# Performance work log

Hardware: AMD Instinct MI355X
Metric: run time of the kernel (lower is better)

Reference implementation:

```python
import jax, jax.numpy as jnp
import numpy as np

NUM_HEADS = 16
NUM_LANDMARKS = 64
N_ITER = 6


def iterative_inv(mat):
    # mat: (B, H, L, L) row-stochastic kernel; Newton-Schulz-style iteration
    L = mat.shape[-1]
    I = jnp.eye(L, dtype=mat.dtype)
    K = mat
    # init: V = K^T / max_j(sum_i K_ij)
    denom = jnp.max(jnp.sum(K, axis=-2), axis=-1)[:, :, None, None]
    Vm = (1.0 / denom) * jnp.swapaxes(K, -1, -2)
    for _ in range(N_ITER):
        KV = jnp.matmul(K, Vm)
        Vm = jnp.matmul(0.25 * Vm, 13.0 * I - jnp.matmul(KV, 15.0 * I - jnp.matmul(KV, 7.0 * I - KV)))
    return Vm


def setup_inputs() -> dict:
    key = jax.random.key(0)
    kq, kk, kv = jax.random.split(key, 3)
    B, N, C = 4, 4096, 1024
    return {
        "Q": jax.random.normal(kq, (B, N, C), dtype=jnp.float32),
        "K": jax.random.normal(kk, (B, N, C), dtype=jnp.float32),
        "V": jax.random.normal(kv, (B, N, C), dtype=jnp.float32),
    }


def reference(Q, K, V):
    B, N, C = Q.shape
    H, Lm = NUM_HEADS, NUM_LANDMARKS
    hd = C // H
    scale = hd ** 0.5
    # (B, H, N, hd)
    q = Q.reshape(B, N, H, hd).transpose(0, 2, 1, 3) / scale
    k = K.reshape(B, N, H, hd).transpose(0, 2, 1, 3)
    v = V.reshape(B, N, H, hd).transpose(0, 2, 1, 3)

    # landmark pooling (N divisible by Lm): mean over segments of length N//Lm
    seg = N // Lm
    k_lm = k.reshape(B, H, Lm, seg, hd).mean(axis=-2)  # (B,H,Lm,hd)
    q_lm = q.reshape(B, H, Lm, seg, hd).mean(axis=-2)  # (B,H,Lm,hd)

    kernel_1 = jax.nn.softmax(jnp.einsum('bhnd,bhld->bhnl', q, k_lm), axis=-1)   # (B,H,N,Lm)
    kernel_2 = jax.nn.softmax(jnp.einsum('bhmd,bhld->bhml', q_lm, k_lm), axis=-1)  # (B,H,Lm,Lm)
    kernel_3 = jax.nn.softmax(jnp.einsum('bhld,bhnd->bhln', q_lm, k), axis=-1)   # (B,H,Lm,N)

    out = jnp.matmul(jnp.matmul(kernel_1, iterative_inv(kernel_2)), jnp.matmul(kernel_3, v))
    return out.transpose(0, 2, 1, 3).reshape(B, N, C)
```

## Files before the change

### kernel.cpp

```cpp
#include <hip/hip_runtime.h>
#include <math.h>

#define BB 4
#define NN 4096
#define CC 1024
#define HH 16
#define HD 64
#define LM 64
#define SEG 64
#define BHN (BB*HH)
#define MATP 68
#define MATE (64*MATP)

typedef __attribute__((ext_vector_type(8))) short bf16x8;
typedef __attribute__((ext_vector_type(4))) short s16x4;
typedef __attribute__((ext_vector_type(4))) float f32x4;

__device__ __forceinline__ float shfl_sum16(float v) {
  v += __shfl_xor(v, 1, 16);
  v += __shfl_xor(v, 2, 16);
  v += __shfl_xor(v, 4, 16);
  v += __shfl_xor(v, 8, 16);
  return v;
}

__device__ __forceinline__ void split8(const float* f, bf16x8& hi, bf16x8& lo) {
#pragma unroll
  for (int i = 0; i < 8; ++i) {
    unsigned u = __builtin_bit_cast(unsigned, f[i]);
    float hf = __builtin_bit_cast(float, u & 0xFFFF0000u);
    hi[i] = (short)(u >> 16);
    float l = f[i] - hf;
    unsigned ul = __builtin_bit_cast(unsigned, l);
    lo[i] = (short)(ul >> 16);
  }
}

__device__ __forceinline__ void split4(const float* f, s16x4& hi, s16x4& lo) {
#pragma unroll
  for (int i = 0; i < 4; ++i) {
    unsigned u = __builtin_bit_cast(unsigned, f[i]);
    float hf = __builtin_bit_cast(float, u & 0xFFFF0000u);
    hi[i] = (short)(u >> 16);
    float l = f[i] - hf;
    unsigned ul = __builtin_bit_cast(unsigned, l);
    lo[i] = (short)(ul >> 16);
  }
}

__device__ __forceinline__ int planeAddr(int row, int cd) {
  int B = (row << 7) + (cd << 4);
  return B ^ ((row & 7) << 4);
}
__device__ __forceinline__ bf16x8 ldP(const short* __restrict__ P, int row, int cd) {
  return *(const bf16x8*)((const char*)P + planeAddr(row, cd));
}

__device__ __forceinline__ void xpose4(float x[4], int lane) {
  bool p1 = (lane >> 4) & 1;
  float s0 = p1 ? x[0] : x[1], s1 = p1 ? x[2] : x[3];
  float r0 = __shfl_xor(s0, 16, 64), r1 = __shfl_xor(s1, 16, 64);
  if (p1) { x[0] = r0; x[2] = r1; } else { x[1] = r0; x[3] = r1; }
  bool p2 = (lane >> 5) & 1;
  s0 = p2 ? x[0] : x[2]; s1 = p2 ? x[1] : x[3];
  r0 = __shfl_xor(s0, 32, 64); r1 = __shfl_xor(s1, 32, 64);
  if (p2) { x[0] = r0; x[1] = r1; } else { x[2] = r0; x[3] = r1; }
}

__global__ __launch_bounds__(256) void lm_kernel(
    const float* __restrict__ Q, const float* __restrict__ K,
    float* __restrict__ qlm, float* __restrict__ klm) {
  int bh = blockIdx.y; int b = bh >> 4; int h = bh & 15;
  int tid = threadIdx.x;
  int l = blockIdx.x * 4 + (tid >> 6);
  int d = tid & 63;
  const float* qbase = Q + ((size_t)b*NN + (size_t)l*SEG)*CC + h*HD + d;
  const float* kbase = K + ((size_t)b*NN + (size_t)l*SEG)*CC + h*HD + d;
  float sq = 0.f, sk = 0.f;
#pragma unroll 8
  for (int s = 0; s < SEG; ++s) {
    sq += qbase[(size_t)s*CC];
    sk += kbase[(size_t)s*CC];
  }
  qlm[(size_t)bh*4096 + l*64 + d] = sq * (1.0f/(64.0f*8.0f));
  klm[(size_t)bh*4096 + l*64 + d] = sk * (1.0f/64.0f);
}

__global__ __launch_bounds__(256, 3) void k3v_kernel(
    const float* __restrict__ K, const float* __restrict__ V,
    const float* __restrict__ qlm,
    float* __restrict__ S3, float* __restrict__ ACC3) {
  __shared__ alignas(16) short KEh[64*64], KEl[64*64];
  __shared__ alignas(16) short VtH[64*64], VtL[64*64];
  __shared__ alignas(16) float Erow[64*MATP];
  const int bh = blockIdx.y, b = bh >> 4, h = bh & 15;
  const int tile = blockIdx.x, tid = threadIdx.x;
  const int wid = tid >> 6, lane = tid & 63;
  const int lr = lane & 15, lg = lane >> 4;
  const int m0 = wid*16 + lg*4;

  bf16x8 qh[2], ql[2];
#pragma unroll
  for (int ks = 0; ks < 2; ++ks) {
    const float* qp = qlm + (size_t)bh*4096 + (wid*16 + lr)*64 + ks*32 + lg*8;
    float qf[8];
    *(float4*)&qf[0] = *(const float4*)qp;
    *(float4*)&qf[4] = *(const float4*)(qp + 4);
    split8(qf, qh[ks], ql[ks]);
  }

  f32x4 acc2[4];
#pragma unroll
  for (int t = 0; t < 4; ++t) acc2[t] = (f32x4){0.f, 0.f, 0.f, 0.f};
  float srow[4] = {0.f, 0.f, 0.f, 0.f};

  const int rk0 = tid >> 3,        ck = tid & 7;
  const int rk1 = (tid + 256) >> 3;
  const int dV  = 4*lr + lg;

  float4 gk[2][2], gv[4];

#define K3V_LOAD(SUB)                                                          \
  {                                                                            \
    const int n0_ = tile*128 + (SUB)*64;                                       \
    const float* kb0 = &K[((size_t)b*NN + n0_ + rk0)*CC + h*HD + ck*8];        \
    const float* kb1 = &K[((size_t)b*NN + n0_ + rk1)*CC + h*HD + ck*8];        \
    gk[0][0] = *(const float4*)kb0;  gk[0][1] = *(const float4*)(kb0 + 4);     \
    gk[1][0] = *(const float4*)kb1;  gk[1][1] = *(const float4*)(kb1 + 4);     \
    _Pragma("unroll")                                                          \
    for (int q = 0; q < 4; ++q) {                                              \
      int f = tid + 256*q;                                                     \
      int r = f >> 4, c4 = (f & 15) << 2;                                      \
      gv[q] = *(const float4*)&V[((size_t)b*NN + n0_ + r)*CC + h*HD + c4];     \
    }                                                                          \
  }

#define K3V_WRITE()                                                            \
  {                                                                            \
    _Pragma("unroll")                                                          \
    for (int q2 = 0; q2 < 2; ++q2) {                                           \
      float kf[8];                                                             \
      *(float4*)&kf[0] = gk[q2][0];                                            \
      *(float4*)&kf[4] = gk[q2][1];                                            \
      bf16x8 khv, klv; split8(kf, khv, klv);                                   \
      int r = q2 ? rk1 : rk0;                                                  \
      int A = planeAddr(r, ck);                                                \
      *(bf16x8*)((char*)KEh + A) = khv;                                        \
      *(bf16x8*)((char*)KEl + A) = klv;                                        \
    }                                                                          \
    _Pragma("unroll")                                                          \
    for (int q = 0; q < 4; ++q) {                                              \
      float x[4] = {gv[q].x, gv[q].y, gv[q].z, gv[q].w};                       \
      xpose4(x, lane);                                                         \
      int nb = 16*q + 4*wid;                                                   \
      s16x4 vh, vl; split4(x, vh, vl);                                         \
      int B = (dV << 7) + (nb << 1);                                           \
      B ^= (dV & 7) << 4;                                                      \
      *(s16x4*)((char*)VtH + B) = vh;                                          \
      *(s16x4*)((char*)VtL + B) = vl;                                          \
    }                                                                          \
  }

#define K3V_COMPUTE()                                                          \
  {                                                                            \
    f32x4 zacc[4];                                                             \
    _Pragma("unroll")                                                          \
    for (int t = 0; t < 4; ++t) zacc[t] = (f32x4){0.f, 0.f, 0.f, 0.f};        \
    _Pragma("unroll")                                                          \
    for (int ks = 0; ks < 2; ++ks) {                                           \
      _Pragma("unroll")                                                        \
      for (int tn = 0; tn < 4; ++tn) {                                         \
        bf16x8 bh_ = ldP(KEh, tn*16 + lr, 4*ks + lg);                          \
        bf16x8 bl_ = ldP(KEl, tn*16 + lr, 4*ks + lg);                          \
        zacc[tn] = __builtin_amdgcn_mfma_f32_16x16x32_bf16(qh[ks], bh_, zacc[tn], 0, 0, 0); \
        zacc[tn] = __builtin_amdgcn_mfma_f32_16x16x32_bf16(qh[ks], bl_, zacc[tn], 0, 0, 0); \
        zacc[tn] = __builtin_amdgcn_mfma_f32_16x16x32_bf16(ql[ks], bh_, zacc[tn], 0, 0, 0); \
      }                                                                        \
    }                                                                          \
    float e[4][4];                                                             \
    _Pragma("unroll")                                                          \
    for (int tn = 0; tn < 4; ++tn)                                             \
      _Pragma("unroll")                                                        \
      for (int r = 0; r < 4; ++r) e[tn][r] = __expf(zacc[tn][r]);              \
    _Pragma("unroll")                                                          \
    for (int r = 0; r < 4; ++r) {                                              \
      float t = e[0][r] + e[1][r] + e[2][r] + e[3][r];                         \
      srow[r] += shfl_sum16(t);                                                \
    }                                                                          \
    _Pragma("unroll")                                                          \
    for (int tn = 0; tn < 4; ++tn) {                                           \
      const int n = tn*16 + lr;                                                \
      _Pragma("unroll")                                                        \
      for (int r = 0; r < 4; ++r) Erow[(m0 + r)*MATP + n] = e[tn][r];          \
    }                                                                          \
    _Pragma("unroll")                                                          \
    for (int ks = 0; ks < 2; ++ks) {                                           \
      float fa[8];                                                             \
      const float* ap = Erow + (wid*16 + lr)*MATP + ks*32 + lg*8;              \
      *(float4*)&fa[0] = *(const float4*)ap;                                   \
      *(float4*)&fa[4] = *(const float4*)(ap + 4);                             \
      bf16x8 ah, al; split8(fa, ah, al);                                       \
      _Pragma("unroll")                                                        \
      for (int tn = 0; tn < 4; ++tn) {                                         \
        bf16x8 bh_ = ldP(VtH, tn*16 + lr, 4*ks + lg);                          \
        bf16x8 bl_ = ldP(VtL, tn*16 + lr, 4*ks + lg);                          \
        acc2[tn] = __builtin_amdgcn_mfma_f32_16x16x32_bf16(ah, bh_, acc2[tn], 0, 0, 0); \
        acc2[tn] = __builtin_amdgcn_mfma_f32_16x16x32_bf16(ah, bl_, acc2[tn], 0, 0, 0); \
        acc2[tn] = __builtin_amdgcn_mfma_f32_16x16x32_bf16(al, bh_, acc2[tn], 0, 0, 0); \
      }                                                                        \
    }                                                                          \
  }

  K3V_LOAD(0)
  K3V_WRITE()
  __syncthreads();
  K3V_LOAD(1)
  K3V_COMPUTE()
  __syncthreads();
  K3V_WRITE()
  __syncthreads();
  K3V_COMPUTE()

  if (lr == 0) {
#pragma unroll
    for (int r = 0; r < 4; ++r)
      atomicAdd(&S3[bh*64 + m0 + r], srow[r]);
  }
#pragma unroll
  for (int tn = 0; tn < 4; ++tn)
#pragma unroll
    for (int r = 0; r < 4; ++r)
      atomicAdd(&ACC3[(size_t)bh*4096 + (m0 + r)*64 + tn*16 + lr], acc2[tn][r]);
}

template<bool FUSE, bool HR, bool HC, bool HG>
__device__ __forceinline__ void mm_mfma(
    const float* __restrict__ Arow, const float* __restrict__ Scol,
    float diagc, float scale,
    float* __restrict__ OutRow, float* __restrict__ OutCol, float* __restrict__ OutGlob,
    int wr, int tn, int lane) {
  const int lr = lane & 15, lg = lane >> 4;
  f32x4 acc = (f32x4){0.f, 0.f, 0.f, 0.f};

#pragma unroll
  for (int ks = 0; ks < 2; ++ks) {
    const int kb = ks*32 + lg*8;
    float fa[8];
    const float* ap = Arow + (wr*16 + lr)*MATP + kb;
    *(float4*)&fa[0] = *(const float4*)ap;
    *(float4*)&fa[4] = *(const float4*)(ap + 4);
    bf16x8 ah, al; split8(fa, ah, al);
    float fb[8];
    const float* bp = Scol + (tn*16 + lr)*MATP + kb;
    *(float4*)&fb[0] = *(const float4*)bp;
    *(float4*)&fb[4] = *(const float4*)(bp + 4);
    if (FUSE) {
      int diff = (tn*16 + lr) - kb;
#pragma unroll
      for (int i = 0; i < 8; ++i) fb[i] = (i == diff ? diagc : 0.f) - fb[i];
    }
    bf16x8 bh_, bl_; split8(fb, bh_, bl_);
    acc = __builtin_amdgcn_mfma_f32_16x16x32_bf16(ah, bh_, acc, 0, 0, 0);
    acc = __builtin_amdgcn_mfma_f32_16x16x32_bf16(ah, bl_, acc, 0, 0, 0);
    acc = __builtin_amdgcn_mfma_f32_16x16x32_bf16(al, bh_, acc, 0, 0, 0);
  }
  __syncthreads();
  const int n = tn*16 + lr, m0 = wr*16 + lg*4;
  float v0 = scale*acc[0], v1 = scale*acc[1], v2 = scale*acc[2], v3 = scale*acc[3];
  if (HC) *(float4*)&OutCol[n*MATP + m0] = make_float4(v0, v1, v2, v3);
  if (HR) {
    OutRow[(m0+0)*MATP + n] = v0;
    OutRow[(m0+1)*MATP + n] = v1;
    OutRow[(m0+2)*MATP + n] = v2;
    OutRow[(m0+3)*MATP + n] = v3;
  }
  if (HG) {
    OutGlob[(m0+0)*64 + n] = v0;
    OutGlob[(m0+1)*64 + n] = v1;
    OutGlob[(m0+2)*64 + n] = v2;
    OutGlob[(m0+3)*64 + n] = v3;
  }
  __syncthreads();
}

__global__ __launch_bounds__(1024, 1) void inv_kernel(
    const float* __restrict__ qlm, const float* __restrict__ klm,
    const float* __restrict__ S3, const float* __restrict__ ACC3,
    float* __restrict__ W) {
  extern __shared__ float sm[];
  float* K2row = sm;
  float* Vmrow = sm + 1*MATE;
  float* Vmcol = sm + 2*MATE;
  float* Xrow  = sm + 3*MATE;
  float* Xcol  = sm + 4*MATE;
  float* Ycol  = sm + 5*MATE;
  float* Zcol  = sm + 6*MATE;
  float* rs    = sm + 7*MATE;
  float* rinv  = rs + 256;
  float* red   = rinv + 64;
  const int bh = blockIdx.x, tid = threadIdx.x;
  const int wid = tid >> 6, lane = tid & 63;
  const int wr = wid & 3, tn = wid >> 2;
  const int lr = lane & 15, lg = lane >> 4;
  const int m0 = wr*16 + lg*4, n = tn*16 + lr;

  {
    int f = tid, r = f >> 4, c4 = (f & 15) << 2;
    *(float4*)&Xrow[r*MATP + c4] = *(const float4*)&qlm[(size_t)bh*4096 + f*4];
    *(float4*)&Xcol[r*MATP + c4] = *(const float4*)&klm[(size_t)bh*4096 + f*4];
  }
  __syncthreads();

  {
    f32x4 zacc = (f32x4){0.f, 0.f, 0.f, 0.f};
#pragma unroll
    for (int ks = 0; ks < 2; ++ks) {
      const int kb = ks*32 + lg*8;
      float fa[8];
      const float* ap = Xrow + (wr*16 + lr)*MATP + kb;
      *(float4*)&fa[0] = *(const float4*)ap;
      *(float4*)&fa[4] = *(const float4*)(ap + 4);
      bf16x8 ah, al; split8(fa, ah, al);
      float fb[8];
      const float* bp = Xcol + (tn*16 + lr)*MATP + kb;
      *(float4*)&fb[0] = *(const float4*)bp;
      *(float4*)&fb[4] = *(const float4*)(bp + 4);
      bf16x8 bh_, bl_; split8(fb, bh_, bl_);
      zacc = __builtin_amdgcn_mfma_f32_16x16x32_bf16(ah, bh_, zacc, 0, 0, 0);
      zacc = __builtin_amdgcn_mfma_f32_16x16x32_bf16(ah, bl_, zacc, 0, 0, 0);
      zacc = __builtin_amdgcn_mfma_f32_16x16x32_bf16(al, bh_, zacc, 0, 0, 0);
    }
    float e[4];
#pragma unroll
    for (int r = 0; r < 4; ++r) e[r] = __expf(zacc[r]);
    float part[4];
#pragma unroll
    for (int r = 0; r < 4; ++r) part[r] = shfl_sum16(e[r]);
    if (lr == 0) {
#pragma unroll
      for (int r = 0; r < 4; ++r) rs[(m0 + r)*4 + tn] = part[r];
    }
    __syncthreads();
    if (tid < 64)
      rinv[tid] = 1.0f / (rs[tid*4] + rs[tid*4+1] + rs[tid*4+2] + rs[tid*4+3]);
    __syncthreads();
#pragma unroll
    for (int r = 0; r < 4; ++r)
      K2row[(m0+r)*MATP + n] = e[r] * rinv[m0 + r];
  }
  __syncthreads();

  if (tid < 64) {
    float c = 0.f;
#pragma unroll 8
    for (int i = 0; i < 64; ++i) c += K2row[i*MATP + tid];
#pragma unroll
    for (int m = 1; m < 64; m <<= 1) c = fmaxf(c, __shfl_xor(c, m, 64));
    if (tid == 0) red[0] = 1.0f / c;
  }
  __syncthreads();
  const float invden = red[0];

  {
    int f = tid, i = f >> 4, c4 = (f & 15) << 2;
    float4 kv = *(const float4*)&K2row[i*MATP + c4];
    kv.x *= invden; kv.y *= invden; kv.z *= invden; kv.w *= invden;
    *(float4*)&Vmcol[i*MATP + c4] = kv;
    Vmrow[(c4+0)*MATP + i] = kv.x;
    Vmrow[(c4+1)*MATP + i] = kv.y;
    Vmrow[(c4+2)*MATP + i] = kv.z;
    Vmrow[(c4+3)*MATP + i] = kv.w;
  }
  __syncthreads();

  for (int it = 0; it < 6; ++it) {
    mm_mfma<false, true,  true,  false>(K2row, Vmcol, 0.f,  1.0f,  Xrow, Xcol, nullptr, wr, tn, lane);
    mm_mfma<true,  false, true,  false>(Xrow,  Xcol,  7.f,  1.0f,  nullptr, Ycol, nullptr, wr, tn, lane);
    mm_mfma<true,  false, true,  false>(Xrow,  Ycol,  15.f, 1.0f,  nullptr, Zcol, nullptr, wr, tn, lane);
    mm_mfma<true,  true,  true,  false>(Vmrow, Zcol,  13.f, 0.25f, Vmrow, Vmcol, nullptr, wr, tn, lane);
  }

  {
    int f = tid, k = f >> 4, c4 = (f & 15) << 2;
    float4 tv = *(const float4*)&ACC3[(size_t)bh*4096 + f*4];
    float ri = 1.0f / S3[bh*64 + k];
    Ycol[(c4+0)*MATP + k] = tv.x * ri;
    Ycol[(c4+1)*MATP + k] = tv.y * ri;
    Ycol[(c4+2)*MATP + k] = tv.z * ri;
    Ycol[(c4+3)*MATP + k] = tv.w * ri;
  }
  __syncthreads();
  mm_mfma<false, false, false, true>(Vmrow, Ycol, 0.f, 1.0f, nullptr, nullptr, W + (size_t)bh*4096, wr, tn, lane);
}

__global__ __launch_bounds__(256, 3) void out_kernel(
    const float* __restrict__ Q, const float* __restrict__ klm,
    const float* __restrict__ W, float* __restrict__ Out) {
  __shared__ alignas(16) short KlH[64*64], KlL[64*64];
  __shared__ alignas(16) short WtH[64*64], WtL[64*64];
  __shared__ alignas(16) float Prow[64*MATP];
  const int bh = blockIdx.y, b = bh >> 4, h = bh & 15;
  const int n0 = blockIdx.x * 64;
  const int tid = threadIdx.x;
  const int wid = tid >> 6, lane = tid & 63;
  const int lr = lane & 15, lg = lane >> 4;
  const int m0 = wid*16 + lg*4;

#pragma unroll
  for (int q2 = 0; q2 < 2; ++q2) {
    int f = tid + 256*q2;
    int r = f >> 3, c = f & 7;
    const float* kp = &klm[(size_t)bh*4096 + r*64 + c*8];
    float kf[8];
    *(float4*)&kf[0] = *(const float4*)kp;
    *(float4*)&kf[4] = *(const float4*)(kp + 4);
    bf16x8 khv, klv; split8(kf, khv, klv);
    int A = planeAddr(r, c);
    *(bf16x8*)((char*)KlH + A) = khv;
    *(bf16x8*)((char*)KlL + A) = klv;
  }
  const int dW = 4*lr + lg;
#pragma unroll
  for (int q = 0; q < 4; ++q) {
    int f = tid + 256*q;
    int r = f >> 4, c4 = (f & 15) << 2;
    float4 wv = *(const float4*)&W[(size_t)bh*4096 + r*64 + c4];
    float x[4] = {wv.x, wv.y, wv.z, wv.w};
    xpose4(x, lane);
    int nb = 16*q + 4*wid;
    s16x4 wh, wl; split4(x, wh, wl);
    int B = (dW << 7) + (nb << 1);
    B ^= (dW & 7) << 4;
    *(s16x4*)((char*)WtH + B) = wh;
    *(s16x4*)((char*)WtL + B) = wl;
  }

  bf16x8 qh[2], qlo[2];
#pragma unroll
  for (int ks = 0; ks < 2; ++ks) {
    const float* qp = Q + ((size_t)b*NN + n0 + wid*16 + lr)*CC + h*HD + ks*32 + lg*8;
    float qf[8];
    *(float4*)&qf[0] = *(const float4*)qp;
    *(float4*)&qf[4] = *(const float4*)(qp + 4);
#pragma unroll
    for (int i = 0; i < 8; ++i) qf[i] *= 0.125f;
    split8(qf, qh[ks], qlo[ks]);
  }
  __syncthreads();

  f32x4 zacc[4];
#pragma unroll
  for (int t = 0; t < 4; ++t) zacc[t] = (f32x4){0.f, 0.f, 0.f, 0.f};
#pragma unroll
  for (int ks = 0; ks < 2; ++ks) {
#pragma unroll
    for (int tn = 0; tn < 4; ++tn) {
      bf16x8 bh_ = ldP(KlH, tn*16 + lr, 4*ks + lg);
      bf16x8 bl_ = ldP(KlL, tn*16 + lr, 4*ks + lg);
      zacc[tn] = __builtin_amdgcn_mfma_f32_16x16x32_bf16(qh[ks], bh_, zacc[tn], 0, 0, 0);
      zacc[tn] = __builtin_amdgcn_mfma_f32_16x16x32_bf16(qh[ks], bl_, zacc[tn], 0, 0, 0);
      zacc[tn] = __builtin_amdgcn_mfma_f32_16x16x32_bf16(qlo[ks], bh_, zacc[tn], 0, 0, 0);
    }
  }
  float e[4][4];
#pragma unroll
  for (int tn = 0; tn < 4; ++tn)
#pragma unroll
    for (int r = 0; r < 4; ++r) e[tn][r] = __expf(zacc[tn][r]);
#pragma unroll
  for (int r = 0; r < 4; ++r) {
    float t = e[0][r] + e[1][r] + e[2][r] + e[3][r];
    t = shfl_sum16(t);
    float ri = 1.0f / t;
#pragma unroll
    for (int tn = 0; tn < 4; ++tn) e[tn][r] *= ri;
  }
#pragma unroll
  for (int tn = 0; tn < 4; ++tn) {
    const int n = tn*16 + lr;
#pragma unroll
    for (int r = 0; r < 4; ++r) Prow[(m0+r)*MATP + n] = e[tn][r];
  }

  f32x4 oacc[4];
#pragma unroll
  for (int t = 0; t < 4; ++t) oacc[t] = (f32x4){0.f, 0.f, 0.f, 0.f};
#pragma unroll
  for (int ks = 0; ks < 2; ++ks) {
    float fa[8];
    const float* ap = Prow + (wid*16 + lr)*MATP + ks*32 + lg*8;
    *(float4*)&fa[0] = *(const float4*)ap;
    *(float4*)&fa[4] = *(const float4*)(ap + 4);
    bf16x8 ah, al; split8(fa, ah, al);
#pragma unroll
    for (int tn = 0; tn < 4; ++tn) {
      bf16x8 bh_ = ldP(WtH, tn*16 + lr, 4*ks + lg);
      bf16x8 bl_ = ldP(WtL, tn*16 + lr, 4*ks + lg);
      oacc[tn] = __builtin_amdgcn_mfma_f32_16x16x32_bf16(ah, bh_, oacc[tn], 0, 0, 0);
      oacc[tn] = __builtin_amdgcn_mfma_f32_16x16x32_bf16(ah, bl_, oacc[tn], 0, 0, 0);
      oacc[tn] = __builtin_amdgcn_mfma_f32_16x16x32_bf16(al, bh_, oacc[tn], 0, 0, 0);
    }
  }
#pragma unroll
  for (int tn = 0; tn < 4; ++tn) {
    const int d = tn*16 + lr;
#pragma unroll
    for (int r = 0; r < 4; ++r)
      Out[((size_t)b*NN + n0 + m0 + r)*CC + h*HD + d] = oacc[tn][r];
  }
}

extern "C" void kernel_launch(void* const* d_in, const int* in_sizes, int n_in,
                              void* d_out, int out_size, void* d_ws, size_t ws_size,
                              hipStream_t stream) {
  const float* Q = (const float*)d_in[0];
  const float* K = (const float*)d_in[1];
  const float* V = (const float*)d_in[2];
  float* out = (float*)d_out;
  float* ws  = (float*)d_ws;

  float* qlm  = ws;
  float* klm  = ws + 262144;
  float* S3   = ws + 524288;
  float* ACC3 = ws + 528384;
  float* Wm   = ws + 790528;

  size_t shC = (size_t)(7*MATE + 384)*sizeof(float);
  hipFuncSetAttribute((const void*)inv_kernel,
                      hipFuncAttributeMaxDynamicSharedMemorySize, (int)shC);

  hipMemsetAsync(S3, 0, (4096 + 262144)*sizeof(float), stream);

  lm_kernel <<<dim3(16, BHN), 256, 0, stream>>>(Q, K, qlm, klm);
  k3v_kernel<<<dim3(32, BHN), 256, 0, stream>>>(K, V, qlm, S3, ACC3);
  inv_kernel<<<dim3(BHN),    1024, shC, stream>>>(qlm, klm, S3, ACC3, Wm);
  out_kernel<<<dim3(64, BHN), 256, 0, stream>>>(Q, klm, Wm, out);
}
```

Measured before the change: 141.0 us.

## Fuse K landmark pooling into k3v kernel and read K fragments directly from global

Landmark pooling of K moves out of the separate pooling kernel and into k3v_kernel. Wave 0 accumulates K rows while it loads them as MFMA B-fragments straight from global memory, so K is read from HBM once instead of twice. K and klm are no longer staged through LDS in k3v and out kernels, which frees shared memory and lets launch bounds rise to 4 blocks per CU. The costs are more redundant global loads per wave (every wave reloads K tiles), a shuffle reduction in wave 0, and the unrolled 64-row segment now maps exactly onto each 64-row subtile.

After: 159.6 us. 1.13x slower.

```diff
diff --git a/kernel.cpp b/kernel.cpp
--- a/kernel.cpp
+++ b/kernel.cpp
@@ -24,6 +24,10 @@
   return v;
 }
 
+#define F4ADD(a, b) { (a).x += (b).x; (a).y += (b).y; (a).z += (b).z; (a).w += (b).w; }
+#define RSUM16(a) { (a).x = shfl_sum16((a).x); (a).y = shfl_sum16((a).y); \
+                    (a).z = shfl_sum16((a).z); (a).w = shfl_sum16((a).w); }
+
 __device__ __forceinline__ void split8(const float* f, bf16x8& hi, bf16x8& lo) {
 #pragma unroll
   for (int i = 0; i < 8; ++i) {
@@ -67,30 +71,23 @@
   if (p2) { x[0] = r0; x[1] = r1; } else { x[2] = r0; x[3] = r1; }
 }
 
-__global__ __launch_bounds__(256) void lm_kernel(
-    const float* __restrict__ Q, const float* __restrict__ K,
-    float* __restrict__ qlm, float* __restrict__ klm) {
+__global__ __launch_bounds__(256) void lm_q_kernel(
+    const float* __restrict__ Q, float* __restrict__ qlm) {
   int bh = blockIdx.y; int b = bh >> 4; int h = bh & 15;
   int tid = threadIdx.x;
   int l = blockIdx.x * 4 + (tid >> 6);
   int d = tid & 63;
   const float* qbase = Q + ((size_t)b*NN + (size_t)l*SEG)*CC + h*HD + d;
-  const float* kbase = K + ((size_t)b*NN + (size_t)l*SEG)*CC + h*HD + d;
-  float sq = 0.f, sk = 0.f;
+  float sq = 0.f;
 #pragma unroll 8
-  for (int s = 0; s < SEG; ++s) {
-    sq += qbase[(size_t)s*CC];
-    sk += kbase[(size_t)s*CC];
-  }
+  for (int s = 0; s < SEG; ++s) sq += qbase[(size_t)s*CC];
   qlm[(size_t)bh*4096 + l*64 + d] = sq * (1.0f/(64.0f*8.0f));
-  klm[(size_t)bh*4096 + l*64 + d] = sk * (1.0f/64.0f);
-}
-
-__global__ __launch_bounds__(256, 3) void k3v_kernel(
+}
+
+__global__ __launch_bounds__(256, 4) void k3v_kernel(
     const float* __restrict__ K, const float* __restrict__ V,
-    const float* __restrict__ qlm,
+    const float* __restrict__ qlm, float* __restrict__ klm,
     float* __restrict__ S3, float* __restrict__ ACC3) {
-  __shared__ alignas(16) short KEh[64*64], KEl[64*64];
   __shared__ alignas(16) short VtH[64*64], VtL[64*64];
   __shared__ alignas(16) float Erow[64*MATP];
   const int bh = blockIdx.y, b = bh >> 4, h = bh & 15;
@@ -98,6 +95,7 @@
   const int wid = tid >> 6, lane = tid & 63;
   const int lr = lane & 15, lg = lane >> 4;
   const int m0 = wid*16 + lg*4;
+  const int dV = 4*lr + lg;
 
   bf16x8 qh[2], ql[2];
 #pragma unroll
@@ -113,20 +111,11 @@
 #pragma unroll
   for (int t = 0; t < 4; ++t) acc2[t] = (f32x4){0.f, 0.f, 0.f, 0.f};
   float srow[4] = {0.f, 0.f, 0.f, 0.f};
-
-  const int rk0 = tid >> 3,        ck = tid & 7;
-  const int rk1 = (tid + 256) >> 3;
-  const int dV  = 4*lr + lg;
-
-  float4 gk[2][2], gv[4];
-
-#define K3V_LOAD(SUB)                                                          \
+  float4 gv[4];
+
+#define K3V_VLOAD(SUB)                                                         \
   {                                                                            \
     const int n0_ = tile*128 + (SUB)*64;                                       \
-    const float* kb0 = &K[((size_t)b*NN + n0_ + rk0)*CC + h*HD + ck*8];        \
-    const float* kb1 = &K[((size_t)b*NN + n0_ + rk1)*CC + h*HD + ck*8];        \
-    gk[0][0] = *(const float4*)kb0;  gk[0][1] = *(const float4*)(kb0 + 4);     \
-    gk[1][0] = *(const float4*)kb1;  gk[1][1] = *(const float4*)(kb1 + 4);     \
     _Pragma("unroll")                                                          \
     for (int q = 0; q < 4; ++q) {                                              \
       int f = tid + 256*q;                                                     \
@@ -135,19 +124,8 @@
     }                                                                          \
   }
 
-#define K3V_WRITE()                                                            \
+#define K3V_VWRITE()                                                           \
   {                                                                            \
-    _Pragma("unroll")                                                          \
-    for (int q2 = 0; q2 < 2; ++q2) {                                           \
-      float kf[8];                                                             \
-      *(float4*)&kf[0] = gk[q2][0];                                            \
-      *(float4*)&kf[4] = gk[q2][1];                                            \
-      bf16x8 khv, klv; split8(kf, khv, klv);                                   \
-      int r = q2 ? rk1 : rk0;                                                  \
-      int A = planeAddr(r, ck);                                                \
-      *(bf16x8*)((char*)KEh + A) = khv;                                        \
-      *(bf16x8*)((char*)KEl + A) = klv;                                        \
-    }                                                                          \
     _Pragma("unroll")                                                          \
     for (int q = 0; q < 4; ++q) {                                              \
       float x[4] = {gv[q].x, gv[q].y, gv[q].z, gv[q].w};                       \
@@ -161,21 +139,32 @@
     }                                                                          \
   }
 
-#define K3V_COMPUTE()                                                          \
+#define K3V_GEMM1(SUB)                                                         \
   {                                                                            \
+    const int n0_ = tile*128 + (SUB)*64;                                       \
     f32x4 zacc[4];                                                             \
     _Pragma("unroll")                                                          \
     for (int t = 0; t < 4; ++t) zacc[t] = (f32x4){0.f, 0.f, 0.f, 0.f};        \
-    _Pragma("unroll")                                                          \
-    for (int ks = 0; ks < 2; ++ks) {                                           \
-      _Pragma("unroll")                                                        \
-      for (int tn = 0; tn < 4; ++tn) {                                         \
-        bf16x8 bh_ = ldP(KEh, tn*16 + lr, 4*ks + lg);                          \
-        bf16x8 bl_ = ldP(KEl, tn*16 + lr, 4*ks + lg);                          \
-        zacc[tn] = __builtin_amdgcn_mfma_f32_16x16x32_bf16(qh[ks], bh_, zacc[tn], 0, 0, 0); \
-        zacc[tn] = __builtin_amdgcn_mfma_f32_16x16x32_bf16(qh[ks], bl_, zacc[tn], 0, 0, 0); \
-        zacc[tn] = __builtin_amdgcn_mfma_f32_16x16x32_bf16(ql[ks], bh_, zacc[tn], 0, 0, 0); \
-      }                                                                        \
+    float4 ksA = make_float4(0.f,0.f,0.f,0.f), ksB = ksA, ksC = ksA, ksD = ksA;\
+    _Pragma("unroll")                                                          \
+    for (int tn = 0; tn < 4; ++tn) {                                           \
+      const float* kp = &K[(size_t)(b*NN + n0_ + tn*16 + lr)*CC + h*HD + lg*8];\
+      float4 k00 = *(const float4*)kp;                                         \
+      float4 k01 = *(const float4*)(kp + 4);                                   \
+      float4 k10 = *(const float4*)(kp + 32);                                  \
+      float4 k11 = *(const float4*)(kp + 36);                                  \
+      if (wid == 0) { F4ADD(ksA,k00) F4ADD(ksB,k01) F4ADD(ksC,k10) F4ADD(ksD,k11) } \
+      float kf[8];                                                             \
+      *(float4*)&kf[0] = k00; *(float4*)&kf[4] = k01;                          \
+      bf16x8 b0h, b0l; split8(kf, b0h, b0l);                                   \
+      *(float4*)&kf[0] = k10; *(float4*)&kf[4] = k11;                          \
+      bf16x8 b1h, b1l; split8(kf, b1h, b1l);                                   \
+      zacc[tn] = __builtin_amdgcn_mfma_f32_16x16x32_bf16(qh[0], b0h, zacc[tn], 0, 0, 0); \
+      zacc[tn] = __builtin_amdgcn_mfma_f32_16x16x32_bf16(qh[0], b0l, zacc[tn], 0, 0, 0); \
+      zacc[tn] = __builtin_amdgcn_mfma_f32_16x16x32_bf16(ql[0], b0h, zacc[tn], 0, 0, 0); \
+      zacc[tn] = __builtin_amdgcn_mfma_f32_16x16x32_bf16(qh[1], b1h, zacc[tn], 0, 0, 0); \
+      zacc[tn] = __builtin_amdgcn_mfma_f32_16x16x32_bf16(qh[1], b1l, zacc[tn], 0, 0, 0); \
+      zacc[tn] = __builtin_amdgcn_mfma_f32_16x16x32_bf16(ql[1], b1h, zacc[tn], 0, 0, 0); \
     }                                                                          \
     float e[4][4];                                                             \
     _Pragma("unroll")                                                          \
@@ -193,6 +182,21 @@
       _Pragma("unroll")                                                        \
       for (int r = 0; r < 4; ++r) Erow[(m0 + r)*MATP + n] = e[tn][r];          \
     }                                                                          \
+    if (wid == 0) {                                                            \
+      RSUM16(ksA) RSUM16(ksB) RSUM16(ksC) RSUM16(ksD)                          \
+      if (lr == 0) {                                                           \
+        float* kr = klm + (size_t)bh*4096 + (tile*2 + (SUB))*64;               \
+        const float s_ = 1.0f/64.0f;                                           \
+        *(float4*)(kr + lg*8)          = make_float4(ksA.x*s_, ksA.y*s_, ksA.z*s_, ksA.w*s_); \
+        *(float4*)(kr + lg*8 + 4)      = make_float4(ksB.x*s_, ksB.y*s_, ksB.z*s_, ksB.w*s_); \
+        *(float4*)(kr + 32 + lg*8)     = make_float4(ksC.x*s_, ksC.y*s_, ksC.z*s_, ksC.w*s_); \
+        *(float4*)(kr + 32 + lg*8 + 4) = make_float4(ksD.x*s_, ksD.y*s_, ksD.z*s_, ksD.w*s_); \
+      }                                                                        \
+    }                                                                          \
+  }
+
+#define K3V_GEMM2()                                                            \
+  {                                                                            \
     _Pragma("unroll")                                                          \
     for (int ks = 0; ks < 2; ++ks) {                                           \
       float fa[8];                                                             \
@@ -211,15 +215,17 @@
     }                                                                          \
   }
 
-  K3V_LOAD(0)
-  K3V_WRITE()
-  __syncthreads();
-  K3V_LOAD(1)
-  K3V_COMPUTE()
-  __syncthreads();
-  K3V_WRITE()
-  __syncthreads();
-  K3V_COMPUTE()
+  K3V_VLOAD(0)
+  K3V_VWRITE()
+  K3V_VLOAD(1)
+  K3V_GEMM1(0)
+  __syncthreads();
+  K3V_GEMM2()
+  __syncthreads();
+  K3V_VWRITE()
+  K3V_GEMM1(1)
+  __syncthreads();
+  K3V_GEMM2()
 
   if (lr == 0) {
 #pragma unroll
@@ -393,10 +399,9 @@
   mm_mfma<false, false, false, true>(Vmrow, Ycol, 0.f, 1.0f, nullptr, nullptr, W + (size_t)bh*4096, wr, tn, lane);
 }
 
-__global__ __launch_bounds__(256, 3) void out_kernel(
+__global__ __launch_bounds__(256, 4) void out_kernel(
     const float* __restrict__ Q, const float* __restrict__ klm,
     const float* __restrict__ W, float* __restrict__ Out) {
-  __shared__ alignas(16) short KlH[64*64], KlL[64*64];
   __shared__ alignas(16) short WtH[64*64], WtL[64*64];
   __shared__ alignas(16) float Prow[64*MATP];
   const int bh = blockIdx.y, b = bh >> 4, h = bh & 15;
@@ -406,19 +411,6 @@
   const int lr = lane & 15, lg = lane >> 4;
   const int m0 = wid*16 + lg*4;
 
-#pragma unroll
-  for (int q2 = 0; q2 < 2; ++q2) {
-    int f = tid + 256*q2;
-    int r = f >> 3, c = f & 7;
-    const float* kp = &klm[(size_t)bh*4096 + r*64 + c*8];
-    float kf[8];
-    *(float4*)&kf[0] = *(const float4*)kp;
-    *(float4*)&kf[4] = *(const float4*)(kp + 4);
-    bf16x8 khv, klv; split8(kf, khv, klv);
-    int A = planeAddr(r, c);
-    *(bf16x8*)((char*)KlH + A) = khv;
-    *(bf16x8*)((char*)KlL + A) = klv;
-  }
   const int dW = 4*lr + lg;
 #pragma unroll
   for (int q = 0; q < 4; ++q) {
@@ -446,21 +438,28 @@
     for (int i = 0; i < 8; ++i) qf[i] *= 0.125f;
     split8(qf, qh[ks], qlo[ks]);
   }
-  __syncthreads();
 
   f32x4 zacc[4];
 #pragma unroll
   for (int t = 0; t < 4; ++t) zacc[t] = (f32x4){0.f, 0.f, 0.f, 0.f};
 #pragma unroll
-  for (int ks = 0; ks < 2; ++ks) {
-#pragma unroll
-    for (int tn = 0; tn < 4; ++tn) {
-      bf16x8 bh_ = ldP(KlH, tn*16 + lr, 4*ks + lg);
-      bf16x8 bl_ = ldP(KlL, tn*16 + lr, 4*ks + lg);
-      zacc[tn] = __builtin_amdgcn_mfma_f32_16x16x32_bf16(qh[ks], bh_, zacc[tn], 0, 0, 0);
-      zacc[tn] = __builtin_amdgcn_mfma_f32_16x16x32_bf16(qh[ks], bl_, zacc[tn], 0, 0, 0);
-      zacc[tn] = __builtin_amdgcn_mfma_f32_16x16x32_bf16(qlo[ks], bh_, zacc[tn], 0, 0, 0);
-    }
+  for (int tn = 0; tn < 4; ++tn) {
+    const float* kp = &klm[(size_t)bh*4096 + (tn*16 + lr)*64 + lg*8];
+    float4 k00 = *(const float4*)kp;
+    float4 k01 = *(const float4*)(kp + 4);
+    float4 k10 = *(const float4*)(kp + 32);
+    float4 k11 = *(const float4*)(kp + 36);
+    float kf[8];
+    *(float4*)&kf[0] = k00; *(float4*)&kf[4] = k01;
+    bf16x8 b0h, b0l; split8(kf, b0h, b0l);
+    *(float4*)&kf[0] = k10; *(float4*)&kf[4] = k11;
+    bf16x8 b1h, b1l; split8(kf, b1h, b1l);
+    zacc[tn] = __builtin_amdgcn_mfma_f32_16x16x32_bf16(qh[0], b0h, zacc[tn], 0, 0, 0);
+    zacc[tn] = __builtin_amdgcn_mfma_f32_16x16x32_bf16(qh[0], b0l, zacc[tn], 0, 0, 0);
+    zacc[tn] = __builtin_amdgcn_mfma_f32_16x16x32_bf16(qlo[0], b0h, zacc[tn], 0, 0, 0);
+    zacc[tn] = __builtin_amdgcn_mfma_f32_16x16x32_bf16(qh[1], b1h, zacc[tn], 0, 0, 0);
+    zacc[tn] = __builtin_amdgcn_mfma_f32_16x16x32_bf16(qh[1], b1l, zacc[tn], 0, 0, 0);
+    zacc[tn] = __builtin_amdgcn_mfma_f32_16x16x32_bf16(qlo[1], b1h, zacc[tn], 0, 0, 0);
   }
   float e[4][4];
 #pragma unroll
@@ -481,6 +480,7 @@
 #pragma unroll
     for (int r = 0; r < 4; ++r) Prow[(m0+r)*MATP + n] = e[tn][r];
   }
+  __syncthreads();
 
   f32x4 oacc[4];
 #pragma unroll
@@ -531,8 +531,8 @@
 
   hipMemsetAsync(S3, 0, (4096 + 262144)*sizeof(float), stream);
 
-  lm_kernel <<<dim3(16, BHN), 256, 0, stream>>>(Q, K, qlm, klm);
-  k3v_kernel<<<dim3(32, BHN), 256, 0, stream>>>(K, V, qlm, S3, ACC3);
-  inv_kernel<<<dim3(BHN),    1024, shC, stream>>>(qlm, klm, S3, ACC3, Wm);
-  out_kernel<<<dim3(64, BHN), 256, 0, stream>>>(Q, klm, Wm, out);
-}
+  lm_q_kernel<<<dim3(16, BHN), 256, 0, stream>>>(Q, qlm);
+  k3v_kernel <<<dim3(32, BHN), 256, 0, stream>>>(K, V, qlm, klm, S3, ACC3);
+  inv_kernel <<<dim3(BHN),    1024, shC, stream>>>(qlm, klm, S3, ACC3, Wm);
+  out_kernel <<<dim3(64, BHN), 256, 0, stream>>>(Q, klm, Wm, out);
+}
```

## Replace atomic accumulation with per-tile partials plus reduce kernel; load landmarks directly in out_kernel

Applied to the files above, without the earlier changes.

The k3v kernel now writes per-tile partial sums (numerators and row sums) to a workspace buffer instead of using global atomicAdd. A new reduce kernel sums the 32 partials, which also removes the memset. Separately, out_kernel no longer stages the landmark keys in shared memory: each lane loads and splits its key fragments directly from global memory, which drops one barrier and some LDS and lets occupancy rise to 4 blocks. The cost is an extra kernel launch, extra partial-buffer traffic, and redundant global reads of klm across waves.

New measurement: 150.5 us. 1.07x slower.

```diff
diff --git a/kernel.cpp b/kernel.cpp
--- a/kernel.cpp
+++ b/kernel.cpp
@@ -11,6 +11,8 @@
 #define BHN (BB*HH)
 #define MATP 68
 #define MATE (64*MATP)
+#define NTILE 32
+#define APROW 4160
 
 typedef __attribute__((ext_vector_type(8))) short bf16x8;
 typedef __attribute__((ext_vector_type(4))) short s16x4;
@@ -88,8 +90,7 @@
 
 __global__ __launch_bounds__(256, 3) void k3v_kernel(
     const float* __restrict__ K, const float* __restrict__ V,
-    const float* __restrict__ qlm,
-    float* __restrict__ S3, float* __restrict__ ACC3) {
+    const float* __restrict__ qlm, float* __restrict__ ACC3p) {
   __shared__ alignas(16) short KEh[64*64], KEl[64*64];
   __shared__ alignas(16) short VtH[64*64], VtL[64*64];
   __shared__ alignas(16) float Erow[64*MATP];
@@ -221,16 +222,33 @@
   __syncthreads();
   K3V_COMPUTE()
 
+  float* accp = ACC3p + ((size_t)tile*BHN + bh)*APROW;
   if (lr == 0) {
 #pragma unroll
+    for (int r = 0; r < 4; ++r) accp[4096 + m0 + r] = srow[r];
+  }
+#pragma unroll
+  for (int tn = 0; tn < 4; ++tn)
+#pragma unroll
     for (int r = 0; r < 4; ++r)
-      atomicAdd(&S3[bh*64 + m0 + r], srow[r]);
-  }
-#pragma unroll
-  for (int tn = 0; tn < 4; ++tn)
-#pragma unroll
-    for (int r = 0; r < 4; ++r)
-      atomicAdd(&ACC3[(size_t)bh*4096 + (m0 + r)*64 + tn*16 + lr], acc2[tn][r]);
+      accp[(m0 + r)*64 + tn*16 + lr] = acc2[tn][r];
+}
+
+__global__ __launch_bounds__(256) void reduce_kernel(
+    const float* __restrict__ ACC3p, float* __restrict__ ACC3, float* __restrict__ S3) {
+  const int bh = blockIdx.y;
+  const int f4 = blockIdx.x*256 + threadIdx.x;
+  if (f4 >= APROW/4) return;
+  float4 s = make_float4(0.f, 0.f, 0.f, 0.f);
+  const float* base = ACC3p + (size_t)bh*APROW + f4*4;
+#pragma unroll 4
+  for (int t = 0; t < NTILE; ++t) {
+    float4 v = *(const float4*)(base + (size_t)t*BHN*APROW);
+    s.x += v.x; s.y += v.y; s.z += v.z; s.w += v.w;
+  }
+  const int f = f4*4;
+  if (f < 4096) *(float4*)&ACC3[(size_t)bh*4096 + f] = s;
+  else          *(float4*)&S3[bh*64 + (f - 4096)] = s;
 }
 
 template<bool FUSE, bool HR, bool HC, bool HG>
@@ -393,10 +411,9 @@
   mm_mfma<false, false, false, true>(Vmrow, Ycol, 0.f, 1.0f, nullptr, nullptr, W + (size_t)bh*4096, wr, tn, lane);
 }
 
-__global__ __launch_bounds__(256, 3) void out_kernel(
+__global__ __launch_bounds__(256, 4) void out_kernel(
     const float* __restrict__ Q, const float* __restrict__ klm,
     const float* __restrict__ W, float* __restrict__ Out) {
-  __shared__ alignas(16) short KlH[64*64], KlL[64*64];
   __shared__ alignas(16) short WtH[64*64], WtL[64*64];
   __shared__ alignas(16) float Prow[64*MATP];
   const int bh = blockIdx.y, b = bh >> 4, h = bh & 15;
@@ -406,19 +423,6 @@
   const int lr = lane & 15, lg = lane >> 4;
   const int m0 = wid*16 + lg*4;
 
-#pragma unroll
-  for (int q2 = 0; q2 < 2; ++q2) {
-    int f = tid + 256*q2;
-    int r = f >> 3, c = f & 7;
-    const float* kp = &klm[(size_t)bh*4096 + r*64 + c*8];
-    float kf[8];
-    *(float4*)&kf[0] = *(const float4*)kp;
-    *(float4*)&kf[4] = *(const float4*)(kp + 4);
-    bf16x8 khv, klv; split8(kf, khv, klv);
-    int A = planeAddr(r, c);
-    *(bf16x8*)((char*)KlH + A) = khv;
-    *(bf16x8*)((char*)KlL + A) = klv;
-  }
   const int dW = 4*lr + lg;
 #pragma unroll
   for (int q = 0; q < 4; ++q) {
@@ -446,21 +450,28 @@
     for (int i = 0; i < 8; ++i) qf[i] *= 0.125f;
     split8(qf, qh[ks], qlo[ks]);
   }
-  __syncthreads();
 
   f32x4 zacc[4];
 #pragma unroll
   for (int t = 0; t < 4; ++t) zacc[t] = (f32x4){0.f, 0.f, 0.f, 0.f};
 #pragma unroll
-  for (int ks = 0; ks < 2; ++ks) {
-#pragma unroll
-    for (int tn = 0; tn < 4; ++tn) {
-      bf16x8 bh_ = ldP(KlH, tn*16 + lr, 4*ks + lg);
-      bf16x8 bl_ = ldP(KlL, tn*16 + lr, 4*ks + lg);
-      zacc[tn] = __builtin_amdgcn_mfma_f32_16x16x32_bf16(qh[ks], bh_, zacc[tn], 0, 0, 0);
-      zacc[tn] = __builtin_amdgcn_mfma_f32_16x16x32_bf16(qh[ks], bl_, zacc[tn], 0, 0, 0);
-      zacc[tn] = __builtin_amdgcn_mfma_f32_16x16x32_bf16(qlo[ks], bh_, zacc[tn], 0, 0, 0);
-    }
+  for (int tn = 0; tn < 4; ++tn) {
+    const float* kp = &klm[(size_t)bh*4096 + (tn*16 + lr)*64 + lg*8];
+    float4 k00 = *(const float4*)kp;
+    float4 k01 = *(const float4*)(kp + 4);
+    float4 k10 = *(const float4*)(kp + 32);
+    float4 k11 = *(const float4*)(kp + 36);
+    float kf[8];
+    *(float4*)&kf[0] = k00; *(float4*)&kf[4] = k01;
+    bf16x8 b0h, b0l; split8(kf, b0h, b0l);
+    *(float4*)&kf[0] = k10; *(float4*)&kf[4] = k11;
+    bf16x8 b1h, b1l; split8(kf, b1h, b1l);
+    zacc[tn] = __builtin_amdgcn_mfma_f32_16x16x32_bf16(qh[0], b0h, zacc[tn], 0, 0, 0);
+    zacc[tn] = __builtin_amdgcn_mfma_f32_16x16x32_bf16(qh[0], b0l, zacc[tn], 0, 0, 0);
+    zacc[tn] = __builtin_amdgcn_mfma_f32_16x16x32_bf16(qlo[0], b0h, zacc[tn], 0, 0, 0);
+    zacc[tn] = __builtin_amdgcn_mfma_f32_16x16x32_bf16(qh[1], b1h, zacc[tn], 0, 0, 0);
+    zacc[tn] = __builtin_amdgcn_mfma_f32_16x16x32_bf16(qh[1], b1l, zacc[tn], 0, 0, 0);
+    zacc[tn] = __builtin_amdgcn_mfma_f32_16x16x32_bf16(qlo[1], b1h, zacc[tn], 0, 0, 0);
   }
   float e[4][4];
 #pragma unroll
@@ -481,6 +492,7 @@
 #pragma unroll
     for (int r = 0; r < 4; ++r) Prow[(m0+r)*MATP + n] = e[tn][r];
   }
+  __syncthreads();
 
   f32x4 oacc[4];
 #pragma unroll
@@ -519,20 +531,20 @@
   float* out = (float*)d_out;
   float* ws  = (float*)d_ws;
 
-  float* qlm  = ws;
-  float* klm  = ws + 262144;
-  float* S3   = ws + 524288;
-  float* ACC3 = ws + 528384;
-  float* Wm   = ws + 790528;
+  float* qlm   = ws;
+  float* klm   = ws + 262144;
+  float* S3    = ws + 524288;
+  float* ACC3  = ws + 528384;
+  float* Wm    = ws + 790528;
+  float* ACC3p = ws + 1052672;
 
   size_t shC = (size_t)(7*MATE + 384)*sizeof(float);
   hipFuncSetAttribute((const void*)inv_kernel,
                       hipFuncAttributeMaxDynamicSharedMemorySize, (int)shC);
 
-  hipMemsetAsync(S3, 0, (4096 + 262144)*sizeof(float), stream);
-
-  lm_kernel <<<dim3(16, BHN), 256, 0, stream>>>(Q, K, qlm, klm);
-  k3v_kernel<<<dim3(32, BHN), 256, 0, stream>>>(K, V, qlm, S3, ACC3);
-  inv_kernel<<<dim3(BHN),    1024, shC, stream>>>(qlm, klm, S3, ACC3, Wm);
-  out_kernel<<<dim3(64, BHN), 256, 0, stream>>>(Q, klm, Wm, out);
-}
+  lm_kernel    <<<dim3(16, BHN), 256, 0, stream>>>(Q, K, qlm, klm);
+  k3v_kernel   <<<dim3(NTILE, BHN), 256, 0, stream>>>(K, V, qlm, ACC3p);
+  reduce_kernel<<<dim3(5, BHN), 256, 0, stream>>>(ACC3p, ACC3, S3);
+  inv_kernel   <<<dim3(BHN),    1024, shC, stream>>>(qlm, klm, S3, ACC3, Wm);
+  out_kernel   <<<dim3(64, BHN), 256, 0, stream>>>(Q, klm, Wm, out);
+}
```
